# Kernel optimization log

Measured on AMD Instinct MI355X. Metric: run time of the kernel, lower is better.

## Reference

```python
import jax, jax.numpy as jnp
import numpy as np

B, S, D = 4, 2048, 1024
D_K, D_V = 1024, 1024


def setup_inputs() -> dict:
    key = jax.random.key(0)
    ks = jax.random.split(key, 9)
    s = 1.0 / np.sqrt(D)
    return {
        "q_in": jax.random.normal(ks[0], (B, S, D), jnp.float32),
        "k_in": jax.random.normal(ks[1], (B, S, D), jnp.float32),
        "v_in": jax.random.normal(ks[2], (B, S, D), jnp.float32),
        "Wq": jax.random.normal(ks[3], (D, D_K), jnp.float32) * s,
        "bq": jnp.zeros((D_K,), jnp.float32),
        "Wk": jax.random.normal(ks[4], (D, D_K), jnp.float32) * s,
        "bk": jnp.zeros((D_K,), jnp.float32),
        "Wv": jax.random.normal(ks[5], (D, D_V), jnp.float32) * s,
        "bv": jnp.zeros((D_V,), jnp.float32),
    }


def reference(q_in, k_in, v_in, Wq, bq, Wk, bk, Wv, bv):
    q = jnp.einsum("bsd,dk->bsk", q_in, Wq) + bq  # [B,S,d_k]
    k = jnp.einsum("bsd,dk->bsk", k_in, Wk) + bk  # [B,S,d_k]
    v = jnp.einsum("bsd,dv->bsv", v_in, Wv) + bv  # [B,S,d_v]
    scores = jnp.einsum("bqk,bsk->bqs", q, k) / jnp.sqrt(jnp.float32(D_K))
    attn = jax.nn.softmax(scores, axis=-1)  # [B,S,S]
    return jnp.einsum("bqs,bsv->bqv", attn, v)
```

## Files before the change

kernel.cpp:

```cpp
#include <hip/hip_runtime.h>
#include <stdint.h>

#define B_  4
#define S_  2048
#define D_  1024
#define DK_ 1024
#define DV_ 1024

typedef __attribute__((ext_vector_type(8)))  short short8;
typedef __attribute__((ext_vector_type(16))) float floatx16;

#define ASYNC16(gsrc, ldst)                                                        \
  __builtin_amdgcn_global_load_lds(                                                \
      (const __attribute__((address_space(1))) unsigned int*)(gsrc),               \
      (__attribute__((address_space(3))) unsigned int*)(ldst), 16, 0, 0)

__device__ __forceinline__ unsigned short f2bf(float f) {
  union { float f; uint32_t u; } v; v.f = f;
  uint32_t r = v.u + 0x7fffu + ((v.u >> 16) & 1u);
  return (unsigned short)(r >> 16);
}

__global__ __launch_bounds__(256)
void prep(const float* __restrict__ q, const float* __restrict__ k, const float* __restrict__ v,
          const float* __restrict__ W0, const float* __restrict__ W1, const float* __restrict__ W2,
          unsigned short* __restrict__ qkv, unsigned short* __restrict__ WT) {
  const int bid = blockIdx.x, tid = threadIdx.x;
  if (bid < 12288) {
    const int t  = bid >> 12;
    const int cb = bid & 4095;
    const float* in = (t == 0) ? q : (t == 1) ? k : v;
    unsigned short* o = qkv + (long)t * ((long)B_ * S_ * D_);
    const int i0 = cb * 512 + tid;
    float4 v0 = ((const float4*)in)[i0];
    float4 v1 = ((const float4*)in)[i0 + 256];
    ushort4 u0, u1;
    u0.x = f2bf(v0.x); u0.y = f2bf(v0.y); u0.z = f2bf(v0.z); u0.w = f2bf(v0.w);
    u1.x = f2bf(v1.x); u1.y = f2bf(v1.y); u1.z = f2bf(v1.z); u1.w = f2bf(v1.w);
    ((ushort4*)o)[i0] = u0;
    ((ushort4*)o)[i0 + 256] = u1;
  } else {
    const int b2 = bid - 12288;
    const int w  = b2 >> 10;
    const int tl = b2 & 1023;
    const float* in = (w == 0) ? W0 : (w == 1) ? W1 : W2;
    unsigned short* o = WT + (long)w * D_ * DK_;
    __shared__ float tile[32][33];
    const int bx = (tl & 31) * 32, by = (tl >> 5) * 32;
    const int tx = tid & 31, ty = tid >> 5;
    for (int r = ty; r < 32; r += 8)
      tile[r][tx] = in[(long)(by + r) * DK_ + bx + tx];
    __syncthreads();
    for (int r = ty; r < 32; r += 8)
      o[(long)(bx + r) * D_ + by + tx] = f2bf(tile[tx][r]);
  }
}

__device__ __forceinline__ void storeC(float* p, float v)          { *p = v; }
__device__ __forceinline__ void storeC(unsigned short* p, float v) { *p = f2bf(v); }

template <typename OutT, int NOUT, int MODE>
__global__ __launch_bounds__(256)
void gemm_bt32(const unsigned short* __restrict__ A0, const unsigned short* __restrict__ A1,
               const unsigned short* __restrict__ A2, const unsigned short* __restrict__ Bm,
               OutT* __restrict__ C0, OutT* __restrict__ C1, OutT* __restrict__ C2,
               const float* __restrict__ b0, const float* __restrict__ b1,
               const float* __restrict__ b2, float* __restrict__ rowsum,
               int N, int K, long sA, long sB, long sC, float scale) {
  __shared__ __align__(16) unsigned short As[2][128 * 32];
  __shared__ __align__(16) unsigned short Bs[2][128 * 32];
  __shared__ float invs[128];
  const int tid  = threadIdx.x;
  const int lane = tid & 63, wave = tid >> 6;
  const int wm = (wave >> 1) * 64, wn = (wave & 1) * 64;
  const int lm = lane & 31;
  const int hi = lane >> 5;
  const long zb = blockIdx.z;
  const int m0  = blockIdx.y * 128;
  const int n0g = blockIdx.x * 128;

  const unsigned short* A = A0;
  OutT* C = C0;
  const float* bias = b0;
  int n0 = n0g, sel = 0;
  if (NOUT == 3) {
    sel = n0g >> 10;
    n0 = n0g & 1023;
    if (sel == 1)      { A = A1; C = C1; bias = b1; }
    else if (sel == 2) { A = A2; C = C2; bias = b2; }
  }
  A += zb * sA;
  const unsigned short* Bp = Bm + zb * sB;
  C += zb * sC;

  const int rr = lane >> 2;
  const int cc = (((lane & 3) ^ ((lane >> 3) & 3)) * 8);
  const unsigned short* agA = A  + (long)(m0  + 16 * wave + rr) * K + cc;
  const unsigned short* agB = Bp + (long)(n0g + 16 * wave + rr) * K + cc;
  const unsigned short* ag0 = agA;
  const unsigned short* ag1 = agA + 32;
  const unsigned short* ag2 = agA + 64 * (long)K;
  const unsigned short* ag3 = agA + 64 * (long)K + 32;
  const unsigned short* bg0 = agB;
  const unsigned short* bg1 = agB + 32;
  const unsigned short* bg2 = agB + 64 * (long)K;
  const unsigned short* bg3 = agB + 64 * (long)K + 32;
  unsigned short* al0 = &As[0][wave * 512];
  unsigned short* al1 = &As[1][wave * 512];
  unsigned short* al2 = &As[0][(wave + 4) * 512];
  unsigned short* al3 = &As[1][(wave + 4) * 512];
  unsigned short* bl0 = &Bs[0][wave * 512];
  unsigned short* bl1 = &Bs[1][wave * 512];
  unsigned short* bl2 = &Bs[0][(wave + 4) * 512];
  unsigned short* bl3 = &Bs[1][(wave + 4) * 512];

  floatx16 acc[2][2] = {};
  const int sw = (lm >> 1) & 3;

  for (int kt = 0; kt < K; kt += 64) {
    __syncthreads();
    ASYNC16(ag0, al0); ASYNC16(ag1, al1); ASYNC16(ag2, al2); ASYNC16(ag3, al3);
    ASYNC16(bg0, bl0); ASYNC16(bg1, bl1); ASYNC16(bg2, bl2); ASYNC16(bg3, bl3);
    __syncthreads();

#pragma unroll
    for (int s = 0; s < 4; s++) {
      const int h   = s >> 1;
      const int off = (((s & 1) * 2 + hi) ^ sw) * 8;
      short8 af[2], bf[2];
#pragma unroll
      for (int i = 0; i < 2; i++)
        af[i] = *(const short8*)&As[h][(wm + i * 32 + lm) * 32 + off];
#pragma unroll
      for (int j = 0; j < 2; j++)
        bf[j] = *(const short8*)&Bs[h][(wn + j * 32 + lm) * 32 + off];
#pragma unroll
      for (int i = 0; i < 2; i++)
#pragma unroll
        for (int j = 0; j < 2; j++)
          acc[i][j] = __builtin_amdgcn_mfma_f32_32x32x16_bf16(af[i], bf[j], acc[i][j], 0, 0, 0);
    }
    ag0 += 64; ag1 += 64; ag2 += 64; ag3 += 64;
    bg0 += 64; bg1 += 64; bg2 += 64; bg3 += 64;
  }

  if (MODE == 2) {
    __syncthreads();
    if (tid < 128) invs[tid] = 1.0f / rowsum[zb * S_ + m0 + tid];
    __syncthreads();
  }

  if (NOUT == 3 && sel == 2) {
    unsigned short* Vt = (unsigned short*)C;
    const int b = m0 >> 11;
    const int sbase = (m0 & 2047);
#pragma unroll
    for (int i = 0; i < 2; i++) {
      const int srowb = sbase + wm + i * 32 + (hi << 2);
#pragma unroll
      for (int j = 0; j < 2; j++) {
        const int col = n0 + wn + j * 32 + lm;
        const float bv = bias[col];
        unsigned short* vp = Vt + ((long)b * DV_ + col) * S_ + srowb;
#pragma unroll
        for (int g = 0; g < 4; g++) {
          ushort4 u;
          u.x = f2bf(acc[i][j][4 * g + 0] + bv);
          u.y = f2bf(acc[i][j][4 * g + 1] + bv);
          u.z = f2bf(acc[i][j][4 * g + 2] + bv);
          u.w = f2bf(acc[i][j][4 * g + 3] + bv);
          *(ushort4*)(vp + 8 * g) = u;
        }
      }
    }
  } else if (MODE == 1) {
#pragma unroll
    for (int i = 0; i < 2; i++) {
#pragma unroll
      for (int r = 0; r < 16; r++) {
        const int row = m0 + wm + i * 32 + (r & 3) + ((r >> 2) << 3) + (hi << 2);
        float sum2 = 0.f;
#pragma unroll
        for (int j = 0; j < 2; j++) {
          const int col = n0 + wn + j * 32 + lm;
          float e = __expf(acc[i][j][r] * scale);
          storeC(C + (long)row * N + col, e);
          sum2 += e;
        }
#pragma unroll
        for (int msk = 1; msk < 32; msk <<= 1) sum2 += __shfl_xor(sum2, msk, 64);
        if ((lane & 31) == 0) atomicAdd(&rowsum[zb * S_ + row], sum2);
      }
    }
  } else {
#pragma unroll
    for (int i = 0; i < 2; i++) {
#pragma unroll
      for (int j = 0; j < 2; j++) {
        const int col = n0 + wn + j * 32 + lm;
        const float bv = bias ? bias[col] : 0.f;
#pragma unroll
        for (int r = 0; r < 16; r++) {
          const int rl = wm + i * 32 + (r & 3) + ((r >> 2) << 3) + (hi << 2);
          float val = acc[i][j][r] * scale + bv;
          if (MODE == 2) val *= invs[rl];
          storeC(C + (long)(m0 + rl) * N + col, val);
        }
      }
    }
  }
}

extern "C" void kernel_launch(void* const* d_in, const int* in_sizes, int n_in,
                              void* d_out, int out_size, void* d_ws, size_t ws_size,
                              hipStream_t stream) {
  const float* q_in = (const float*)d_in[0];
  const float* k_in = (const float*)d_in[1];
  const float* v_in = (const float*)d_in[2];
  const float* Wq   = (const float*)d_in[3];
  const float* bq   = (const float*)d_in[4];
  const float* Wk   = (const float*)d_in[5];
  const float* bk   = (const float*)d_in[6];
  const float* Wv   = (const float*)d_in[7];
  const float* bv   = (const float*)d_in[8];
  float* out = (float*)d_out;

  char* ws = (char*)d_ws;
  const long nX = (long)B_ * S_ * D_;
  const long nW = (long)D_ * DK_;
  unsigned short* qb  = (unsigned short*)(ws);
  unsigned short* kb  = qb + nX;
  unsigned short* vb  = kb + nX;
  unsigned short* WqT = vb + nX;
  unsigned short* Qb  = WqT + 3 * nW;
  unsigned short* Kb  = Qb + nX;
  unsigned short* Vt  = Kb + nX;
  float*          rowsum = (float*)(Vt + nX);
  unsigned short* U   = (unsigned short*)ws;

  dim3 blk(256);

  hipMemsetAsync(rowsum, 0, (size_t)B_ * S_ * sizeof(float), stream);

  {
    dim3 g(12288 + 3072);
    prep<<<g, blk, 0, stream>>>(q_in, k_in, v_in, Wq, Wk, Wv, qb, WqT);
  }
  {
    dim3 g(3 * DK_ / 128, (B_ * S_) / 128, 1);
    gemm_bt32<unsigned short, 3, 0><<<g, blk, 0, stream>>>(
        qb, kb, vb, WqT, Qb, Kb, Vt, bq, bk, bv, nullptr, DK_, D_, 0, 0, 0, 1.f);
  }
  {
    dim3 g(S_ / 128, S_ / 128, B_);
    gemm_bt32<unsigned short, 1, 1><<<g, blk, 0, stream>>>(
        Qb, nullptr, nullptr, Kb, U, nullptr, nullptr, nullptr, nullptr, nullptr, rowsum,
        S_, DK_, (long)S_ * DK_, (long)S_ * DK_, (long)S_ * S_, 0.03125f);
  }
  {
    dim3 g(DV_ / 128, S_ / 128, B_);
    gemm_bt32<float, 1, 2><<<g, blk, 0, stream>>>(
        U, nullptr, nullptr, Vt, out, nullptr, nullptr, nullptr, nullptr, nullptr, rowsum,
        DV_, S_, (long)S_ * S_, (long)DV_ * S_, (long)S_ * DV_, 1.f);
  }
}
```

Measured before the change: 347.5 us.

## Double-buffer GEMM K-loop with async LDS prefetch and remap blocks across XCDs

The GEMM main loop now loads the next 32-wide K slice into the alternate LDS buffer while MFMAs run on the current one, with one barrier per iteration instead of two. The goal is to hide global-to-LDS latency. Block indices are also remapped so that consecutive logical tiles are spread in strides of eight, aiming at better L2 locality across the XCDs. In exchange, each iteration now covers half as much K, so the loop runs twice as many times. The remap assumes the total block count is divisible by 8.

Result: faster. 335.0 us (-3.6%).

```diff
diff --git a/kernel.cpp b/kernel.cpp
--- a/kernel.cpp
+++ b/kernel.cpp
@@ -75,9 +75,18 @@
   const int wm = (wave >> 1) * 64, wn = (wave & 1) * 64;
   const int lm = lane & 31;
   const int hi = lane >> 5;
-  const long zb = blockIdx.z;
-  const int m0  = blockIdx.y * 128;
-  const int n0g = blockIdx.x * 128;
+
+  const int gx = gridDim.x, gy = gridDim.y;
+  const int T  = gx * gy * (int)gridDim.z;
+  const int l  = blockIdx.x + gx * (blockIdx.y + gy * blockIdx.z);
+  const int l2 = (l & 7) * (T >> 3) + (l >> 3);
+  const int bxi = l2 % gx;
+  const int byi = (l2 / gx) % gy;
+  const int bzi = l2 / (gx * gy);
+
+  const long zb = bzi;
+  const int m0  = byi * 128;
+  const int n0g = bxi * 128;
 
   const unsigned short* A = A0;
   OutT* C = C0;
@@ -95,54 +104,51 @@
 
   const int rr = lane >> 2;
   const int cc = (((lane & 3) ^ ((lane >> 3) & 3)) * 8);
-  const unsigned short* agA = A  + (long)(m0  + 16 * wave + rr) * K + cc;
-  const unsigned short* agB = Bp + (long)(n0g + 16 * wave + rr) * K + cc;
-  const unsigned short* ag0 = agA;
-  const unsigned short* ag1 = agA + 32;
-  const unsigned short* ag2 = agA + 64 * (long)K;
-  const unsigned short* ag3 = agA + 64 * (long)K + 32;
-  const unsigned short* bg0 = agB;
-  const unsigned short* bg1 = agB + 32;
-  const unsigned short* bg2 = agB + 64 * (long)K;
-  const unsigned short* bg3 = agB + 64 * (long)K + 32;
-  unsigned short* al0 = &As[0][wave * 512];
-  unsigned short* al1 = &As[1][wave * 512];
-  unsigned short* al2 = &As[0][(wave + 4) * 512];
-  unsigned short* al3 = &As[1][(wave + 4) * 512];
-  unsigned short* bl0 = &Bs[0][wave * 512];
-  unsigned short* bl1 = &Bs[1][wave * 512];
-  unsigned short* bl2 = &Bs[0][(wave + 4) * 512];
-  unsigned short* bl3 = &Bs[1][(wave + 4) * 512];
+  const unsigned short* gA0 = A  + (long)(m0  + 16 * wave + rr) * K + cc;
+  const unsigned short* gA1 = gA0 + 64 * (long)K;
+  const unsigned short* gB0 = Bp + (long)(n0g + 16 * wave + rr) * K + cc;
+  const unsigned short* gB1 = gB0 + 64 * (long)K;
+  const int la0 = wave * 512, la1 = (wave + 4) * 512;
 
   floatx16 acc[2][2] = {};
   const int sw = (lm >> 1) & 3;
 
-  for (int kt = 0; kt < K; kt += 64) {
-    __syncthreads();
-    ASYNC16(ag0, al0); ASYNC16(ag1, al1); ASYNC16(ag2, al2); ASYNC16(ag3, al3);
-    ASYNC16(bg0, bl0); ASYNC16(bg1, bl1); ASYNC16(bg2, bl2); ASYNC16(bg3, bl3);
-    __syncthreads();
-
-#pragma unroll
-    for (int s = 0; s < 4; s++) {
-      const int h   = s >> 1;
-      const int off = (((s & 1) * 2 + hi) ^ sw) * 8;
-      short8 af[2], bf[2];
-#pragma unroll
-      for (int i = 0; i < 2; i++)
-        af[i] = *(const short8*)&As[h][(wm + i * 32 + lm) * 32 + off];
-#pragma unroll
-      for (int j = 0; j < 2; j++)
-        bf[j] = *(const short8*)&Bs[h][(wn + j * 32 + lm) * 32 + off];
-#pragma unroll
-      for (int i = 0; i < 2; i++)
-#pragma unroll
-        for (int j = 0; j < 2; j++)
-          acc[i][j] = __builtin_amdgcn_mfma_f32_32x32x16_bf16(af[i], bf[j], acc[i][j], 0, 0, 0);
-    }
-    ag0 += 64; ag1 += 64; ag2 += 64; ag3 += 64;
-    bg0 += 64; bg1 += 64; bg2 += 64; bg3 += 64;
-  }
+#define GEMM_COMPUTE(pp)                                                                \
+  _Pragma("unroll")                                                                     \
+  for (int s = 0; s < 2; s++) {                                                         \
+    const int off = ((s * 2 + hi) ^ sw) * 8;                                            \
+    short8 af[2], bf[2];                                                                \
+    _Pragma("unroll")                                                                   \
+    for (int i = 0; i < 2; i++)                                                         \
+      af[i] = *(const short8*)&As[pp][(wm + i * 32 + lm) * 32 + off];                   \
+    _Pragma("unroll")                                                                   \
+    for (int j = 0; j < 2; j++)                                                         \
+      bf[j] = *(const short8*)&Bs[pp][(wn + j * 32 + lm) * 32 + off];                   \
+    _Pragma("unroll")                                                                   \
+    for (int i = 0; i < 2; i++)                                                         \
+      _Pragma("unroll")                                                                 \
+      for (int j = 0; j < 2; j++)                                                       \
+        acc[i][j] = __builtin_amdgcn_mfma_f32_32x32x16_bf16(af[i], bf[j], acc[i][j], 0, 0, 0); \
+  }
+
+  ASYNC16(gA0, &As[0][la0]); ASYNC16(gA1, &As[0][la1]);
+  ASYNC16(gB0, &Bs[0][la0]); ASYNC16(gB1, &Bs[0][la1]);
+  gA0 += 32; gA1 += 32; gB0 += 32; gB1 += 32;
+  __syncthreads();
+
+  const int nk = K >> 5;
+  int p = 0;
+  for (int kt = 0; kt < nk - 1; kt++) {
+    unsigned short* dA = &As[p ^ 1][0];
+    unsigned short* dB = &Bs[p ^ 1][0];
+    ASYNC16(gA0, dA + la0); ASYNC16(gA1, dA + la1);
+    ASYNC16(gB0, dB + la0); ASYNC16(gB1, dB + la1);
+    gA0 += 32; gA1 += 32; gB0 += 32; gB1 += 32;
+    GEMM_COMPUTE(p)
+    __syncthreads();
+    p ^= 1;
+  }
+  GEMM_COMPUTE(p)
 
   if (MODE == 2) {
     __syncthreads();
@@ -209,6 +215,7 @@
       }
     }
   }
+#undef GEMM_COMPUTE
 }
 
 extern "C" void kernel_launch(void* const* d_in, const int* in_sizes, int n_in,
```
